# Kernel optimization log

Measured on AMD Instinct MI355X. Metric: run time of the kernel, lower is better.

Reference implementation:

```python
import jax, jax.numpy as jnp
import numpy as np

D = 128  # embedding dim (hardcoded by nn.Linear(128*2, 1))


def setup_inputs() -> dict:
    key = jax.random.key(0)
    k1, k2, k3, k4 = jax.random.split(key, 4)
    B, T, N = 256, 64, 2048
    targetsentence_emb = jax.random.normal(k1, (B, T, D), dtype=jnp.float32)
    context_emb = jax.random.normal(k2, (B, N, D), dtype=jnp.float32)
    # Linear(2D -> 1): weight [1, 2D], bias [1]. Store as flat vectors.
    W = jax.random.normal(k3, (2 * D,), dtype=jnp.float32) * (1.0 / np.sqrt(2 * D))
    b = jax.random.normal(k4, (1,), dtype=jnp.float32) * 0.01
    return {"targetsentence_emb": targetsentence_emb, "context_emb": context_emb, "W": W, "b": b}


def reference(targetsentence_emb, context_emb, W, b):
    # Decompose concat+Linear: W = [Wt | Wc], both length D.
    Wt, Wc = W[:D], W[D:]
    T = targetsentence_emb.shape[1]
    # score[b, n] = sum_t (Wt . target[b,t] + Wc . ctx[b,n] + bias)
    #            = sum_t(Wt . target[b,t]) + T * (Wc . ctx[b,n] + bias)
    tgt_term = jnp.einsum('btd,d->b', targetsentence_emb, Wt)  # [B]
    ctx_term = jnp.einsum('bnd,d->bn', context_emb, Wc)        # [B, N]
    scores = tgt_term[:, None] + T * (ctx_term + b[0])         # [B, N]
    attention = jax.nn.softmax(scores, axis=1)                 # softmax over context dim
    # einsum 'bnm,bnk->bnk' with m=1 is elementwise broadcast scaling
    return attention[:, :, None] * context_emb                 # [B, N, D]
```

## Files before the change

### kernel.cpp

```cpp
#include <hip/hip_runtime.h>


#define B_DIM 256
#define T_SCALE 64.0f
#define N_DIM 2048
#define D_DIM 128
#define DVEC  (D_DIM / 4)
#define BLOCK 1024

__global__ __launch_bounds__(BLOCK)
void hop_attn_kernel(const float* __restrict__ ctx,
                     const float* __restrict__ W,
                     float* __restrict__ out) {
    const int b    = blockIdx.x;
    const int tid  = threadIdx.x;
    const int wave = tid >> 6;
    const int lane = tid & 63;
    const int sub  = lane & 31;
    const int half = lane >> 5;

    __shared__ float s_scores[N_DIM];
    __shared__ float s_red[16];
    __shared__ float s_bcast[2];

    const float4* ctx4 = (const float4*)(ctx) + (size_t)b * N_DIM * DVEC;
    float4*       out4 = (float4*)(out)       + (size_t)b * N_DIM * DVEC;

    const float4 wc = ((const float4*)(W + D_DIM))[sub];

    for (int it = 0; it < N_DIM / 32; ++it) {
        const int n = it * 32 + wave * 2 + half;
        const float4 v = ctx4[n * DVEC + sub];
        float p = v.x * wc.x + v.y * wc.y + v.z * wc.z + v.w * wc.w;
        #pragma unroll
        for (int m = 1; m < 32; m <<= 1) p += __shfl_xor(p, m, 64);
        if (sub == 0) s_scores[n] = T_SCALE * p;
    }
    __syncthreads();

    float m0 = fmaxf(s_scores[tid], s_scores[tid + BLOCK]);
    #pragma unroll
    for (int m = 1; m < 64; m <<= 1) m0 = fmaxf(m0, __shfl_xor(m0, m, 64));
    if (lane == 0) s_red[wave] = m0;
    __syncthreads();
    if (wave == 0) {
        float v = (lane < 16) ? s_red[lane] : -3.4e38f;
        #pragma unroll
        for (int m = 1; m < 16; m <<= 1) v = fmaxf(v, __shfl_xor(v, m, 64));
        if (lane == 0) s_bcast[0] = v;
    }
    __syncthreads();
    const float gmax = s_bcast[0];

    const float e0 = __expf(s_scores[tid] - gmax);
    const float e1 = __expf(s_scores[tid + BLOCK] - gmax);
    s_scores[tid]         = e0;
    s_scores[tid + BLOCK] = e1;
    float sum = e0 + e1;
    #pragma unroll
    for (int m = 1; m < 64; m <<= 1) sum += __shfl_xor(sum, m, 64);
    if (lane == 0) s_red[wave] = sum;
    __syncthreads();
    if (wave == 0) {
        float v = (lane < 16) ? s_red[lane] : 0.0f;
        #pragma unroll
        for (int m = 1; m < 16; m <<= 1) v += __shfl_xor(v, m, 64);
        if (lane == 0) s_bcast[1] = v;
    }
    __syncthreads();
    const float inv = 1.0f / s_bcast[1];

    #pragma unroll 4
    for (int i = 0; i < (N_DIM * DVEC) / BLOCK; ++i) {
        const int flat = tid + (i << 10);
        const int n    = flat >> 5;
        const float w  = s_scores[n] * inv;
        const float4 v = ctx4[flat];
        float4 r;
        r.x = v.x * w; r.y = v.y * w; r.z = v.z * w; r.w = v.w * w;
        out4[flat] = r;
    }
}

extern "C" void kernel_launch(void* const* d_in, const int* in_sizes, int n_in,
                              void* d_out, int out_size, void* d_ws, size_t ws_size,
                              hipStream_t stream) {
    (void)in_sizes; (void)n_in; (void)d_ws; (void)ws_size; (void)out_size;
    const float* ctx = (const float*)d_in[1];
    const float* W   = (const float*)d_in[2];
    float* out       = (float*)d_out;

    hipLaunchKernelGGL(hop_attn_kernel, dim3(B_DIM), dim3(BLOCK), 0, stream,
                       ctx, W, out);
}
```

Before: 490.0 us.

## Split fused attention kernel into scores, softmax and scale kernels

Replaces the single kernel, which ran one 1024-thread block per batch row, with three kernels. The first computes context scores with a large grid, the second runs the row softmax in a workspace buffer, and the third scales the context with a large grid. The aim is to remove the low parallelism and serialized per-block phases of the one-block-per-batch design and keep all CUs saturated with memory traffic. The cost is two extra launches and a small scores round trip through global memory. The context is still read twice.

Result: faster. 478.9 us (-2.3%).

```diff
diff --git a/kernel.cpp b/kernel.cpp
--- a/kernel.cpp
+++ b/kernel.cpp
@@ -2,94 +2,106 @@
 
 
 #define B_DIM 256
-#define T_SCALE 64.0f
 #define N_DIM 2048
 #define D_DIM 128
 #define DVEC  (D_DIM / 4)
-#define BLOCK 1024
+#define T_SCALE 64.0f
 
-__global__ __launch_bounds__(BLOCK)
-void hop_attn_kernel(const float* __restrict__ ctx,
-                     const float* __restrict__ W,
-                     float* __restrict__ out) {
-    const int b    = blockIdx.x;
+__global__ __launch_bounds__(256)
+void k_scores(const float* __restrict__ ctx, const float* __restrict__ W,
+              float* __restrict__ scores) {
     const int tid  = threadIdx.x;
     const int wave = tid >> 6;
     const int lane = tid & 63;
     const int sub  = lane & 31;
     const int half = lane >> 5;
-
-    __shared__ float s_scores[N_DIM];
-    __shared__ float s_red[16];
-    __shared__ float s_bcast[2];
-
-    const float4* ctx4 = (const float4*)(ctx) + (size_t)b * N_DIM * DVEC;
-    float4*       out4 = (float4*)(out)       + (size_t)b * N_DIM * DVEC;
+    const int r    = blockIdx.x * 8 + wave * 2 + half;
 
     const float4 wc = ((const float4*)(W + D_DIM))[sub];
+    const float4 v  = ((const float4*)ctx)[(size_t)r * DVEC + sub];
+    float p = v.x * wc.x + v.y * wc.y + v.z * wc.z + v.w * wc.w;
+    #pragma unroll
+    for (int m = 1; m < 32; m <<= 1) p += __shfl_xor(p, m, 64);
+    if (sub == 0) scores[r] = T_SCALE * p;
+}
 
-    for (int it = 0; it < N_DIM / 32; ++it) {
-        const int n = it * 32 + wave * 2 + half;
-        const float4 v = ctx4[n * DVEC + sub];
-        float p = v.x * wc.x + v.y * wc.y + v.z * wc.z + v.w * wc.w;
-        #pragma unroll
-        for (int m = 1; m < 32; m <<= 1) p += __shfl_xor(p, m, 64);
-        if (sub == 0) s_scores[n] = T_SCALE * p;
-    }
+__global__ __launch_bounds__(256)
+void k_softmax(float* __restrict__ s) {
+    const int tid  = threadIdx.x;
+    const int wave = tid >> 6;
+    const int lane = tid & 63;
+    float4* row4 = (float4*)(s + (size_t)blockIdx.x * N_DIM);
+
+    __shared__ float red[4];
+    __shared__ float bc[2];
+
+    float4 a = row4[tid];
+    float4 c = row4[tid + 256];
+
+    float m0 = fmaxf(fmaxf(fmaxf(a.x, a.y), fmaxf(a.z, a.w)),
+                     fmaxf(fmaxf(c.x, c.y), fmaxf(c.z, c.w)));
+    #pragma unroll
+    for (int m = 1; m < 64; m <<= 1) m0 = fmaxf(m0, __shfl_xor(m0, m, 64));
+    if (lane == 0) red[wave] = m0;
+    __syncthreads();
+    const float gmax = fmaxf(fmaxf(red[0], red[1]), fmaxf(red[2], red[3]));
+
+    a.x = __expf(a.x - gmax); a.y = __expf(a.y - gmax);
+    a.z = __expf(a.z - gmax); a.w = __expf(a.w - gmax);
+    c.x = __expf(c.x - gmax); c.y = __expf(c.y - gmax);
+    c.z = __expf(c.z - gmax); c.w = __expf(c.w - gmax);
+
+    float sum = a.x + a.y + a.z + a.w + c.x + c.y + c.z + c.w;
+    #pragma unroll
+    for (int m = 1; m < 64; m <<= 1) sum += __shfl_xor(sum, m, 64);
+    if (lane == 0) red[wave] = sum;
+    __syncthreads();
+    const float inv = 1.0f / (red[0] + red[1] + red[2] + red[3]);
+    (void)bc;
+
+    a.x *= inv; a.y *= inv; a.z *= inv; a.w *= inv;
+    c.x *= inv; c.y *= inv; c.z *= inv; c.w *= inv;
+    row4[tid]       = a;
+    row4[tid + 256] = c;
+}
+
+__global__ __launch_bounds__(256)
+void k_scale(const float* __restrict__ ctx, const float* __restrict__ p,
+             float* __restrict__ out) {
+    const int tid = threadIdx.x;
+    const size_t base_row = (size_t)blockIdx.x * 64;
+
+    __shared__ float sp[64];
+    if (tid < 64) sp[tid] = p[base_row + tid];
     __syncthreads();
 
-    float m0 = fmaxf(s_scores[tid], s_scores[tid + BLOCK]);
+    const float4* c4 = (const float4*)ctx + base_row * DVEC;
+    float4*       o4 = (float4*)out       + base_row * DVEC;
+
     #pragma unroll
-    for (int m = 1; m < 64; m <<= 1) m0 = fmaxf(m0, __shfl_xor(m0, m, 64));
-    if (lane == 0) s_red[wave] = m0;
-    __syncthreads();
-    if (wave == 0) {
-        float v = (lane < 16) ? s_red[lane] : -3.4e38f;
-        #pragma unroll
-        for (int m = 1; m < 16; m <<= 1) v = fmaxf(v, __shfl_xor(v, m, 64));
-        if (lane == 0) s_bcast[0] = v;
-    }
-    __syncthreads();
-    const float gmax = s_bcast[0];
-
-    const float e0 = __expf(s_scores[tid] - gmax);
-    const float e1 = __expf(s_scores[tid + BLOCK] - gmax);
-    s_scores[tid]         = e0;
-    s_scores[tid + BLOCK] = e1;
-    float sum = e0 + e1;
-    #pragma unroll
-    for (int m = 1; m < 64; m <<= 1) sum += __shfl_xor(sum, m, 64);
-    if (lane == 0) s_red[wave] = sum;
-    __syncthreads();
-    if (wave == 0) {
-        float v = (lane < 16) ? s_red[lane] : 0.0f;
-        #pragma unroll
-        for (int m = 1; m < 16; m <<= 1) v += __shfl_xor(v, m, 64);
-        if (lane == 0) s_bcast[1] = v;
-    }
-    __syncthreads();
-    const float inv = 1.0f / s_bcast[1];
-
-    #pragma unroll 4
-    for (int i = 0; i < (N_DIM * DVEC) / BLOCK; ++i) {
-        const int flat = tid + (i << 10);
-        const int n    = flat >> 5;
-        const float w  = s_scores[n] * inv;
-        const float4 v = ctx4[flat];
+    for (int i = 0; i < 8; ++i) {
+        const int f = i * 256 + tid;
+        const float w = sp[f >> 5];
+        const float4 v = c4[f];
         float4 r;
         r.x = v.x * w; r.y = v.y * w; r.z = v.z * w; r.w = v.w * w;
-        out4[flat] = r;
+        o4[f] = r;
     }
 }
 
 extern "C" void kernel_launch(void* const* d_in, const int* in_sizes, int n_in,
                               void* d_out, int out_size, void* d_ws, size_t ws_size,
                               hipStream_t stream) {
-    (void)in_sizes; (void)n_in; (void)d_ws; (void)ws_size; (void)out_size;
+    (void)in_sizes; (void)n_in; (void)out_size; (void)ws_size;
     const float* ctx = (const float*)d_in[1];
     const float* W   = (const float*)d_in[2];
     float* out       = (float*)d_out;
+    float* scores    = (float*)d_ws;
 
-    hipLaunchKernelGGL(hop_attn_kernel, dim3(B_DIM), dim3(BLOCK), 0, stream,
-                       ctx, W, out);
+    hipLaunchKernelGGL(k_scores,  dim3(B_DIM * N_DIM / 8), dim3(256), 0, stream,
+                       ctx, W, scores);
+    hipLaunchKernelGGL(k_softmax, dim3(B_DIM),             dim3(256), 0, stream,
+                       scores);
+    hipLaunchKernelGGL(k_scale,   dim3(B_DIM * N_DIM / 64), dim3(256), 0, stream,
+                       ctx, scores, out);
 }
```
